# Kernel tuning notes

Measured on AMD Instinct MI355X. Metric: run time of the kernel, lower is better.

## Reference

```python
import jax, jax.numpy as jnp
import numpy as np

HIDDEN = 2048
NUM_HEADS = 16
HEAD_DIM = HIDDEN // NUM_HEADS


def setup_inputs() -> dict:
    key = jax.random.key(0)
    ks = jax.random.split(key, 10)
    B, S = 2, 2048
    scale = 1.0 / np.sqrt(HIDDEN)
    inp = {
        "x": jax.random.normal(ks[0], (B, S, HIDDEN), dtype=jnp.float32),
        "attention_mask": jnp.zeros((B, S), dtype=jnp.float32),
        "Wq": jax.random.normal(ks[1], (HIDDEN, HIDDEN), dtype=jnp.float32) * scale,
        "bq": jnp.zeros((HIDDEN,), dtype=jnp.float32),
        "Wk": jax.random.normal(ks[2], (HIDDEN, HIDDEN), dtype=jnp.float32) * scale,
        "bk": jnp.zeros((HIDDEN,), dtype=jnp.float32),
        "Wv": jax.random.normal(ks[3], (HIDDEN, HIDDEN), dtype=jnp.float32) * scale,
        "bv": jnp.zeros((HIDDEN,), dtype=jnp.float32),
        "Wo": jax.random.normal(ks[4], (HIDDEN, HIDDEN), dtype=jnp.float32) * scale,
        "bo": jnp.zeros((HIDDEN,), dtype=jnp.float32),
    }
    return inp


def _split_heads(t):
    # [B, S, H*D] -> [B, H, S, D]
    B, S, _ = t.shape
    return t.reshape(B, S, NUM_HEADS, HEAD_DIM).transpose(0, 2, 1, 3)


def reference(x, attention_mask, Wq, bq, Wk, bk, Wv, bv, Wo, bo):
    B, S, _ = x.shape
    # Linear layers: y = x @ W^T + b (torch nn.Linear convention)
    q = _split_heads(x @ Wq.T + bq)  # [B, H, S, D]
    k = _split_heads(x @ Wk.T + bk)
    v = _split_heads(x @ Wv.T + bv)
    scale = 1.0 / jnp.sqrt(jnp.asarray(HEAD_DIM, dtype=x.dtype))
    scores = jnp.einsum("bhqd,bhkd->bhqk", q, k) * scale  # [B, H, S, S]
    scores = scores + attention_mask[:, None, None, :]  # additive mask broadcast
    attn = jax.nn.softmax(scores, axis=-1)
    out = jnp.einsum("bhqk,bhkd->bhqd", attn, v)  # [B, H, S, D]
    out = out.transpose(0, 2, 1, 3).reshape(B, S, HIDDEN)
    return out @ Wo.T + bo
```

## Files before the change

kernel.cpp:

```cpp
#include <hip/hip_runtime.h>
#include <math.h>

constexpr int S_LEN = 2048;
constexpr int HID   = 2048;
constexpr int NH    = 16;
constexpr int HD    = 128;

typedef __attribute__((ext_vector_type(8))) short short8;
typedef __attribute__((ext_vector_type(4))) float floatx4;

static __device__ __forceinline__ ushort f2bf(float f) {
  union { float f; unsigned u; } v; v.f = f;
  unsigned r = (v.u + 0x7fffu + ((v.u >> 16) & 1u)) >> 16;
  return (ushort)r;
}
static __device__ __forceinline__ ushort f2bf_fast(float f) {
  union { float f; unsigned u; } v; v.f = f;
  return (ushort)((v.u + 0x8000u) >> 16);
}

static __device__ __forceinline__ void glds16(const ushort* g, ushort* l) {
  __builtin_amdgcn_global_load_lds(
      (const __attribute__((address_space(1))) void*)g,
      (__attribute__((address_space(3))) void*)l, 16, 0, 0);
}

static __device__ __forceinline__ void barrier_raw() {
  __builtin_amdgcn_s_barrier();
  asm volatile("" ::: "memory");
}

static __device__ __forceinline__ void cvt4(ushort* dst, const float* src, size_t i) {
  const float4 v = ((const float4*)src)[i];
  ushort4 u = {f2bf(v.x), f2bf(v.y), f2bf(v.z), f2bf(v.w)};
  ((ushort4*)dst)[i] = u;
}

__global__ __launch_bounds__(256)
void convert_all(const float* __restrict__ x,
                 const float* __restrict__ wq, const float* __restrict__ wk,
                 const float* __restrict__ wv, const float* __restrict__ wo,
                 ushort* __restrict__ xb, ushort* __restrict__ wqb,
                 ushort* __restrict__ wkb, ushort* __restrict__ wvb,
                 ushort* __restrict__ wob) {
  const size_t gid = blockIdx.x * 256 + threadIdx.x;
  const size_t T = gridDim.x * 256;
  const size_t NX = (size_t)4096 * HID / 4;
  const size_t NW = (size_t)HID * HID / 4;
  for (size_t i = gid; i < NX; i += T) cvt4(xb, x, i);
  for (size_t i = gid; i < NW; i += T) {
    cvt4(wqb, wq, i);
    cvt4(wkb, wk, i);
    cvt4(wvb, wv, i);
    cvt4(wob, wo, i);
  }
}

#define GEMM_PHASE(KC)                                                        \
  {                                                                           \
    short8 af[4], bf[4];                                                      \
    _Pragma("unroll")                                                         \
    for (int mt = 0; mt < 4; ++mt)                                            \
      af[mt] = *(const short8*)(cA + (wm*64 + mt*16 + n16)*64                 \
                                   + ((((KC)*4 + q4) ^ n7) * 8));             \
    _Pragma("unroll")                                                         \
    for (int nt = 0; nt < 4; ++nt)                                            \
      bf[nt] = *(const short8*)(cB + (wn*64 + nt*16 + n16)*64                 \
                                   + ((((KC)*4 + q4) ^ n7) * 8));             \
    barrier_raw();                                                            \
    asm volatile("s_waitcnt lgkmcnt(0)" ::: "memory");                        \
    __builtin_amdgcn_sched_barrier(0);                                        \
    __builtin_amdgcn_s_setprio(1);                                            \
    _Pragma("unroll")                                                         \
    for (int mt = 0; mt < 4; ++mt)                                            \
      _Pragma("unroll")                                                       \
      for (int nt = 0; nt < 4; ++nt)                                          \
        acc[mt][nt] = __builtin_amdgcn_mfma_f32_16x16x32_bf16(                \
            af[mt], bf[nt], acc[mt][nt], 0, 0, 0);                            \
    __builtin_amdgcn_s_setprio(0);                                            \
    barrier_raw();                                                            \
  }

template <bool BF16OUT>
__device__ __forceinline__
void gemm8_core(const ushort* __restrict__ A, const ushort* __restrict__ W,
                const float* __restrict__ bias, void* __restrict__ Cv,
                int m0, int n0) {
  __shared__ __align__(16) ushort lds[49152];
  constexpr int NT = HID / 64;

  const int tid  = threadIdx.x;
  const int lane = tid & 63;
  const int w    = tid >> 6;
  const int wm   = w >> 1, wn = w & 1;
  const int n16  = lane & 15, q4 = lane >> 4;
  const int n7   = n16 & 7;

  const int srow  = lane >> 3;
  const int sslot = lane & 7;
  const int sl    = sslot ^ srow;

  const ushort* asrc[4];
  const ushort* bsrc[2];
  #pragma unroll
  for (int c = 0; c < 4; ++c)
    asrc[c] = A + (size_t)(m0 + c*64 + w*8 + srow) * HID + sl*8;
  #pragma unroll
  for (int c = 0; c < 2; ++c)
    bsrc[c] = W + (size_t)(n0 + c*64 + w*8 + srow) * HID + sl*8;

  ushort* const A0 = lds;
  ushort* const A1 = lds + 16384;
  ushort* const B0 = lds + 32768;
  ushort* const B1 = lds + 40960;
  const int wofs = w * 512;

  floatx4 acc[4][4];
  #pragma unroll
  for (int i = 0; i < 4; ++i)
    #pragma unroll
    for (int j = 0; j < 4; ++j) acc[i][j] = (floatx4)0.f;

  auto stage_tile = [&](int t, ushort* Ab, ushort* Bb) {
    #pragma unroll
    for (int c = 0; c < 4; ++c) glds16(asrc[c] + (size_t)t*64, Ab + c*4096 + wofs);
    #pragma unroll
    for (int c = 0; c < 2; ++c) glds16(bsrc[c] + (size_t)t*64, Bb + c*4096 + wofs);
  };

  stage_tile(0, A0, B0);
  stage_tile(1, A1, B1);
  asm volatile("s_waitcnt vmcnt(6)" ::: "memory");
  barrier_raw();

  for (int t = 0; t < NT; ++t) {
    const ushort* cA = (t & 1) ? A1 : A0;
    const ushort* cB = (t & 1) ? B1 : B0;

    GEMM_PHASE(0)
    GEMM_PHASE(1)

    if (t + 2 < NT) {
      stage_tile(t + 2, (t & 1) ? A1 : A0, (t & 1) ? B1 : B0);
      asm volatile("s_waitcnt vmcnt(6)" ::: "memory");
      barrier_raw();
    } else if (t + 1 < NT) {
      asm volatile("s_waitcnt vmcnt(0)" ::: "memory");
      barrier_raw();
    }
  }

  float bv4[4];
  #pragma unroll
  for (int nt = 0; nt < 4; ++nt) bv4[nt] = bias[n0 + wn*64 + nt*16 + n16];
  #pragma unroll
  for (int mt = 0; mt < 4; ++mt)
    #pragma unroll
    for (int nt = 0; nt < 4; ++nt)
      #pragma unroll
      for (int r = 0; r < 4; ++r) {
        const int row = m0 + wm*64 + mt*16 + q4*4 + r;
        const int col = n0 + wn*64 + nt*16 + n16;
        if (BF16OUT)
          ((ushort*)Cv)[(size_t)row * HID + col] = f2bf(acc[mt][nt][r] + bv4[nt]);
        else
          ((float*)Cv)[(size_t)row * HID + col] = acc[mt][nt][r] + bv4[nt];
      }
}

static __device__ __forceinline__ void tile_coords(int& m0, int& n0) {
  const int id = blockIdx.y * gridDim.x + blockIdx.x;
  const int s  = ((id & 7) << 5) | (id >> 3);
  m0 = (s >> 4) * 256;
  n0 = (s & 15) * 128;
}

__global__ __launch_bounds__(512, 2)
void gemm_qkv(const ushort* __restrict__ xb,
              const ushort* __restrict__ wqb, const ushort* __restrict__ wkb,
              const ushort* __restrict__ wvb,
              const float* __restrict__ bq, const float* __restrict__ bk,
              const float* __restrict__ bv,
              ushort* __restrict__ qb, ushort* __restrict__ kb_, ushort* __restrict__ vb) {
  const ushort* W; const float* bias; ushort* C;
  if (blockIdx.z == 0)      { W = wqb; bias = bq; C = qb;  }
  else if (blockIdx.z == 1) { W = wkb; bias = bk; C = kb_; }
  else                      { W = wvb; bias = bv; C = vb;  }
  int m0, n0; tile_coords(m0, n0);
  gemm8_core<true>(xb, W, bias, C, m0, n0);
}

__global__ __launch_bounds__(512, 2)
void gemm_o(const ushort* __restrict__ ao, const ushort* __restrict__ wob,
            const float* __restrict__ bo, float* __restrict__ out) {
  int m0, n0; tile_coords(m0, n0);
  gemm8_core<false>(ao, wob, bo, out, m0, n0);
}

__global__ __launch_bounds__(256)
void transpose_v(const ushort* __restrict__ vb, ushort* __restrict__ vt) {
  __shared__ ushort T[64][72];
  const int t  = threadIdx.x;
  const int bh = blockIdx.z;
  const int b = bh >> 4, h = bh & 15;
  const int s0 = blockIdx.x * 64;
  const int d0 = blockIdx.y * 64;
  {
    const int r = t >> 2, c = (t & 3) * 16;
    const ushort* src = vb + (size_t)(b*S_LEN + s0 + r)*HID + h*HD + d0 + c;
    *(uint4*)&T[r][c]     = *(const uint4*)src;
    *(uint4*)&T[r][c + 8] = *(const uint4*)(src + 8);
  }
  __syncthreads();
  {
    const int dd = t >> 2, c = (t & 3) * 16;
    ushort tmp[16];
    #pragma unroll
    for (int j = 0; j < 16; ++j) tmp[j] = T[c + j][dd];
    ushort* dst = vt + (size_t)((b*NH + h)*HD + d0 + dd)*S_LEN + s0 + c;
    *(uint4*)dst       = *(uint4*)tmp;
    *(uint4*)(dst + 8) = *(uint4*)(tmp + 8);
  }
}

__global__ __launch_bounds__(256, 2)
void attn_mfma(const ushort* __restrict__ qb, const ushort* __restrict__ kbuf,
               const ushort* __restrict__ vtb, const float* __restrict__ mask,
               ushort* __restrict__ ao) {
  __shared__ __align__(16) ushort SM[25600];

  const int tid  = threadIdx.x;
  const int w    = tid >> 6;
  const int lane = tid & 63;
  const int n16  = lane & 15;
  const int q4   = lane >> 4;
  const int n7   = n16 & 7;
  const int b  = blockIdx.y >> 4;
  const int h  = blockIdx.y & 15;
  const int q0 = blockIdx.x * 128;
  const float scale = 0.08838834764831845f;

  ushort* Ks = SM;
  ushort* Vs = SM + 8192;
  ushort* Pw = SM + 16384 + w * 2304;

  short8 aq[2][4];
  #pragma unroll
  for (int mt = 0; mt < 2; ++mt) {
    const ushort* qrow = qb + (size_t)(b*S_LEN + q0 + w*32 + mt*16 + n16)*HID + h*HD;
    #pragma unroll
    for (int kc = 0; kc < 4; ++kc)
      aq[mt][kc] = *(const short8*)(qrow + kc*32 + q4*8);
  }

  const ushort* ksrc[4];
  const ushort* vsrc[4];
  #pragma unroll
  for (int i = 0; i < 4; ++i) {
    const int p = (w*4 + i)*64 + lane;
    { const int rho = p >> 4, pc = p & 15;
      const int cl = (pc & 8) | ((pc ^ rho) & 7);
      ksrc[i] = kbuf + (size_t)(b*S_LEN + rho)*HID + h*HD + cl*8; }
    { const int rho = p >> 3, pc = p & 7;
      const int cl = (pc ^ rho) & 7;
      vsrc[i] = vtb + ((size_t)(b*NH + h)*HD + rho)*S_LEN + cl*8; }
  }

  floatx4 oacc[2][8];
  float lp[2][4];
  #pragma unroll
  for (int mt = 0; mt < 2; ++mt) {
    #pragma unroll
    for (int dt = 0; dt < 8; ++dt) oacc[mt][dt] = (floatx4)0.f;
    #pragma unroll
    for (int r = 0; r < 4; ++r) lp[mt][r] = 0.f;
  }

  #pragma unroll
  for (int i = 0; i < 4; ++i) glds16(ksrc[i], Ks + (w*4 + i)*512);
  #pragma unroll
  for (int i = 0; i < 4; ++i) glds16(vsrc[i], Vs + (w*4 + i)*512);

  for (int kb0 = 0; kb0 < S_LEN; kb0 += 64) {
    const int knext = (kb0 + 64 < S_LEN) ? kb0 + 64 : kb0;

    asm volatile("s_waitcnt vmcnt(4)" ::: "memory");
    barrier_raw();

    float mk[4];
    #pragma unroll
    for (int nt = 0; nt < 4; ++nt)
      mk[nt] = mask[(size_t)b*S_LEN + kb0 + nt*16 + n16];

    floatx4 acc[2][4];
    #pragma unroll
    for (int mt = 0; mt < 2; ++mt)
      #pragma unroll
      for (int nt = 0; nt < 4; ++nt) acc[mt][nt] = (floatx4)0.f;
    __builtin_amdgcn_s_setprio(1);
    #pragma unroll
    for (int nt = 0; nt < 4; ++nt) {
      #pragma unroll
      for (int kc = 0; kc < 4; ++kc) {
        const int cl = kc*4 + q4;
        const int pc = (cl & 8) | ((cl ^ n7) & 7);
        const short8 bk = *(const short8*)&Ks[(nt*16 + n16)*128 + pc*8];
        acc[0][nt] = __builtin_amdgcn_mfma_f32_16x16x32_bf16(aq[0][kc], bk, acc[0][nt], 0, 0, 0);
        acc[1][nt] = __builtin_amdgcn_mfma_f32_16x16x32_bf16(aq[1][kc], bk, acc[1][nt], 0, 0, 0);
      }
    }
    __builtin_amdgcn_s_setprio(0);

    barrier_raw();
    #pragma unroll
    for (int i = 0; i < 4; ++i)
      glds16(ksrc[i] + (size_t)knext * HID, Ks + (w*4 + i)*512);

    #pragma unroll
    for (int mt = 0; mt < 2; ++mt)
      #pragma unroll
      for (int r = 0; r < 4; ++r) {
        float p[4];
        #pragma unroll
        for (int nt = 0; nt < 4; ++nt) p[nt] = __expf(acc[mt][nt][r] * scale + mk[nt]);
        lp[mt][r] += (p[0] + p[1]) + (p[2] + p[3]);
        #pragma unroll
        for (int nt = 0; nt < 4; ++nt)
          Pw[(mt*16 + q4*4 + r)*72 + nt*16 + n16] = f2bf_fast(p[nt]);
      }

    asm volatile("s_waitcnt vmcnt(4)" ::: "memory");
    barrier_raw();

    __builtin_amdgcn_s_setprio(1);
    #pragma unroll
    for (int kc2 = 0; kc2 < 2; ++kc2) {
      const short8 ap0 = *(const short8*)&Pw[(0*16 + n16)*72 + kc2*32 + q4*8];
      const short8 ap1 = *(const short8*)&Pw[(1*16 + n16)*72 + kc2*32 + q4*8];
      const int clb = kc2*4 + q4;
      const int pcb = (clb ^ n7) & 7;
      #pragma unroll
      for (int dt = 0; dt < 8; ++dt) {
        const short8 bvf = *(const short8*)&Vs[(dt*16 + n16)*64 + pcb*8];
        oacc[0][dt] = __builtin_amdgcn_mfma_f32_16x16x32_bf16(ap0, bvf, oacc[0][dt], 0, 0, 0);
        oacc[1][dt] = __builtin_amdgcn_mfma_f32_16x16x32_bf16(ap1, bvf, oacc[1][dt], 0, 0, 0);
      }
    }
    __builtin_amdgcn_s_setprio(0);

    barrier_raw();
    #pragma unroll
    for (int i = 0; i < 4; ++i)
      glds16(vsrc[i] + knext, Vs + (w*4 + i)*512);
  }

  #pragma unroll
  for (int mt = 0; mt < 2; ++mt)
    #pragma unroll
    for (int r = 0; r < 4; ++r) {
      float l = lp[mt][r];
      l += __shfl_xor(l, 1);
      l += __shfl_xor(l, 2);
      l += __shfl_xor(l, 4);
      l += __shfl_xor(l, 8);
      lp[mt][r] = 1.0f / l;
    }

  __syncthreads();
  ushort* dump = SM + w * 4352;
  #pragma unroll
  for (int mt = 0; mt < 2; ++mt)
    #pragma unroll
    for (int r = 0; r < 4; ++r) {
      const int row = mt*16 + q4*4 + r;
      #pragma unroll
      for (int dt = 0; dt < 8; ++dt)
        dump[row*136 + dt*16 + n16] = f2bf(oacc[mt][dt][r] * lp[mt][r]);
    }
  const int drow = lane >> 1, dhalf = lane & 1;
  const size_t gbase = (size_t)(b*S_LEN + q0 + w*32 + drow)*HID + h*HD + dhalf*64;
  #pragma unroll
  for (int j = 0; j < 8; ++j)
    *(uint4*)&ao[gbase + j*8] = *(const uint4*)&dump[drow*136 + dhalf*64 + j*8];
}

extern "C" void kernel_launch(void* const* d_in, const int* in_sizes, int n_in,
                              void* d_out, int out_size, void* d_ws, size_t ws_size,
                              hipStream_t stream) {
  (void)n_in; (void)out_size; (void)ws_size;
  const float* x    = (const float*)d_in[0];
  const float* mask = (const float*)d_in[1];
  const float* Wq   = (const float*)d_in[2];
  const float* bq   = (const float*)d_in[3];
  const float* Wk   = (const float*)d_in[4];
  const float* bk   = (const float*)d_in[5];
  const float* Wv   = (const float*)d_in[6];
  const float* bv   = (const float*)d_in[7];
  const float* Wo   = (const float*)d_in[8];
  const float* bo   = (const float*)d_in[9];
  float* out = (float*)d_out;

  const int B = in_sizes[0] / (S_LEN * HID);
  const int M = B * S_LEN;
  const size_t MH = (size_t)M * HID;
  const size_t WW = (size_t)HID * HID;

  ushort* xb   = (ushort*)d_ws;
  ushort* wqb  = xb   + MH;
  ushort* wkb  = wqb  + WW;
  ushort* wvb  = wkb  + WW;
  ushort* wob  = wvb  + WW;
  ushort* qb   = wob  + WW;
  ushort* kbuf = qb   + MH;
  ushort* vb   = kbuf + MH;
  ushort* vt   = vb   + MH;
  ushort* ao   = xb;

  convert_all<<<512, 256, 0, stream>>>(x, Wq, Wk, Wv, Wo, xb, wqb, wkb, wvb, wob);
  gemm_qkv<<<dim3(HID/128, M/256, 3), 512, 0, stream>>>(xb, wqb, wkb, wvb, bq, bk, bv, qb, kbuf, vb);
  transpose_v<<<dim3(S_LEN/64, HD/64, B*NH), 256, 0, stream>>>(vb, vt);
  attn_mfma<<<dim3(S_LEN/128, B*NH), 256, 0, stream>>>(qb, kbuf, vt, mask, ao);
  gemm_o<<<dim3(HID/128, M/256), 512, 0, stream>>>(ao, wob, bo, out);
}
```

Measured before the change: 407.3 us.

## Triple-buffer GEMM LDS tiles with one barrier per K-step

Replaces the double-buffered GEMM main loop, which had four barriers per K tile, with a three-stage LDS ring buffer. Each iteration waits for the current tile, issues one barrier, and then prefetches tile t+2 into the free slot. It then loads both K-halves' fragments and runs all MFMAs. This cuts barrier and synchronisation overhead and lets global loads overlap compute more. In exchange, LDS use rises to 144KB per block, which may reduce occupancy, and fragment registers double.

```diff
diff --git a/kernel.cpp b/kernel.cpp
--- a/kernel.cpp
+++ b/kernel.cpp
@@ -56,37 +56,12 @@
   }
 }
 
-#define GEMM_PHASE(KC)                                                        \
-  {                                                                           \
-    short8 af[4], bf[4];                                                      \
-    _Pragma("unroll")                                                         \
-    for (int mt = 0; mt < 4; ++mt)                                            \
-      af[mt] = *(const short8*)(cA + (wm*64 + mt*16 + n16)*64                 \
-                                   + ((((KC)*4 + q4) ^ n7) * 8));             \
-    _Pragma("unroll")                                                         \
-    for (int nt = 0; nt < 4; ++nt)                                            \
-      bf[nt] = *(const short8*)(cB + (wn*64 + nt*16 + n16)*64                 \
-                                   + ((((KC)*4 + q4) ^ n7) * 8));             \
-    barrier_raw();                                                            \
-    asm volatile("s_waitcnt lgkmcnt(0)" ::: "memory");                        \
-    __builtin_amdgcn_sched_barrier(0);                                        \
-    __builtin_amdgcn_s_setprio(1);                                            \
-    _Pragma("unroll")                                                         \
-    for (int mt = 0; mt < 4; ++mt)                                            \
-      _Pragma("unroll")                                                       \
-      for (int nt = 0; nt < 4; ++nt)                                          \
-        acc[mt][nt] = __builtin_amdgcn_mfma_f32_16x16x32_bf16(                \
-            af[mt], bf[nt], acc[mt][nt], 0, 0, 0);                            \
-    __builtin_amdgcn_s_setprio(0);                                            \
-    barrier_raw();                                                            \
-  }
-
 template <bool BF16OUT>
 __device__ __forceinline__
 void gemm8_core(const ushort* __restrict__ A, const ushort* __restrict__ W,
                 const float* __restrict__ bias, void* __restrict__ Cv,
                 int m0, int n0) {
-  __shared__ __align__(16) ushort lds[49152];
+  __shared__ __align__(16) ushort lds[73728];
   constexpr int NT = HID / 64;
 
   const int tid  = threadIdx.x;
@@ -109,10 +84,6 @@
   for (int c = 0; c < 2; ++c)
     bsrc[c] = W + (size_t)(n0 + c*64 + w*8 + srow) * HID + sl*8;
 
-  ushort* const A0 = lds;
-  ushort* const A1 = lds + 16384;
-  ushort* const B0 = lds + 32768;
-  ushort* const B1 = lds + 40960;
   const int wofs = w * 512;
 
   floatx4 acc[4][4];
@@ -121,32 +92,50 @@
     #pragma unroll
     for (int j = 0; j < 4; ++j) acc[i][j] = (floatx4)0.f;
 
-  auto stage_tile = [&](int t, ushort* Ab, ushort* Bb) {
-    #pragma unroll
-    for (int c = 0; c < 4; ++c) glds16(asrc[c] + (size_t)t*64, Ab + c*4096 + wofs);
-    #pragma unroll
-    for (int c = 0; c < 2; ++c) glds16(bsrc[c] + (size_t)t*64, Bb + c*4096 + wofs);
+  auto stage_tile = [&](int t, ushort* base) {
+    #pragma unroll
+    for (int c = 0; c < 4; ++c)
+      glds16(asrc[c] + (size_t)t*64, base + c*4096 + wofs);
+    #pragma unroll
+    for (int c = 0; c < 2; ++c)
+      glds16(bsrc[c] + (size_t)t*64, base + 16384 + c*4096 + wofs);
   };
 
-  stage_tile(0, A0, B0);
-  stage_tile(1, A1, B1);
-  asm volatile("s_waitcnt vmcnt(6)" ::: "memory");
-  barrier_raw();
+  stage_tile(0, lds);
+  stage_tile(1, lds + 24576);
 
   for (int t = 0; t < NT; ++t) {
-    const ushort* cA = (t & 1) ? A1 : A0;
-    const ushort* cB = (t & 1) ? B1 : B0;
-
-    GEMM_PHASE(0)
-    GEMM_PHASE(1)
-
-    if (t + 2 < NT) {
-      stage_tile(t + 2, (t & 1) ? A1 : A0, (t & 1) ? B1 : B0);
-      asm volatile("s_waitcnt vmcnt(6)" ::: "memory");
-      barrier_raw();
-    } else if (t + 1 < NT) {
-      asm volatile("s_waitcnt vmcnt(0)" ::: "memory");
-      barrier_raw();
+    if (t == NT - 1) asm volatile("s_waitcnt vmcnt(0)" ::: "memory");
+    else             asm volatile("s_waitcnt vmcnt(6)" ::: "memory");
+    barrier_raw();
+
+    if (t + 2 < NT) stage_tile(t + 2, lds + (size_t)((t + 2) % 3) * 24576);
+
+    const ushort* cA = lds + (size_t)(t % 3) * 24576;
+    const ushort* cB = cA + 16384;
+
+    short8 af[2][4], bf[2][4];
+    #pragma unroll
+    for (int kc = 0; kc < 2; ++kc) {
+      #pragma unroll
+      for (int mt = 0; mt < 4; ++mt)
+        af[kc][mt] = *(const short8*)(cA + (wm*64 + mt*16 + n16)*64
+                                         + (((kc*4 + q4) ^ n7) * 8));
+      #pragma unroll
+      for (int nt = 0; nt < 4; ++nt)
+        bf[kc][nt] = *(const short8*)(cB + (wn*64 + nt*16 + n16)*64
+                                         + (((kc*4 + q4) ^ n7) * 8));
+    }
+    #pragma unroll
+    for (int kc = 0; kc < 2; ++kc) {
+      __builtin_amdgcn_s_setprio(1);
+      #pragma unroll
+      for (int mt = 0; mt < 4; ++mt)
+        #pragma unroll
+        for (int nt = 0; nt < 4; ++nt)
+          acc[mt][nt] = __builtin_amdgcn_mfma_f32_16x16x32_bf16(
+              af[kc][mt], bf[kc][nt], acc[mt][nt], 0, 0, 0);
+      __builtin_amdgcn_s_setprio(0);
     }
   }
 
```

New measurement: 414.0 us. No clear change (+1.7%).
